# Optimization experiments

Hardware: AMD Instinct MI355X
Metric: run time of the kernel (lower is better)

## Reference

```python
import jax, jax.numpy as jnp
import numpy as np

NU, NM, E, H = 200000, 40000, 2000000, 64


def setup_inputs() -> dict:
    key = jax.random.key(0)
    ks = jax.random.split(key, 16)
    inp = {}
    inp["x_user"] = jnp.arange(NU, dtype=jnp.int32)
    inp["x_movie"] = jnp.arange(NM, dtype=jnp.int32)
    # user->movie ratings and the reverse edge type (same edges, flipped)
    src_u = jax.random.randint(ks[0], (E,), 0, NU, dtype=jnp.int32)
    dst_m = jax.random.randint(ks[1], (E,), 0, NM, dtype=jnp.int32)
    inp["edge_src_um"], inp["edge_dst_um"] = src_u, dst_m
    inp["edge_src_mu"], inp["edge_dst_mu"] = dst_m, src_u
    inp["user_table"] = jax.random.normal(ks[2], (NU, H), dtype=jnp.float32)
    inp["movie_table"] = jax.random.normal(ks[3], (NM, H), dtype=jnp.float32)
    s = 1.0 / np.sqrt(H)
    wnames = ["Wl1_um", "Wr1_um", "Wl1_mu", "Wr1_mu", "Wl2_um", "Wr2_um", "Wl2_mu", "Wr2_mu"]
    for i, n in enumerate(wnames):
        inp[n] = jax.random.uniform(ks[4 + i], (H, H), minval=-s, maxval=s, dtype=jnp.float32)
    for i, n in enumerate(["b1_um", "b1_mu", "b2_um", "b2_mu"]):
        inp[n] = jax.random.uniform(ks[12 + i], (H,), minval=-s, maxval=s, dtype=jnp.float32)
    return inp


def sage_conv(x_src, x_dst, src, dst, Wl, Wr, b, n_dst):
    """PyG SAGEConv (bipartite, aggr='mean'): lin_l(mean_j x_j) + lin_r(x_i) + b."""
    msg = x_src[src]                                            # [E, H] gather
    agg = jax.ops.segment_sum(msg, dst, num_segments=n_dst)     # [n_dst, H]
    cnt = jax.ops.segment_sum(jnp.ones((src.shape[0], 1), x_src.dtype), dst,
                              num_segments=n_dst)
    agg = agg / jnp.maximum(cnt, 1.0)                           # mean, 0 for isolated nodes
    return agg @ Wl + x_dst @ Wr + b


def reference(x_user, x_movie, edge_src_um, edge_dst_um, edge_src_mu, edge_dst_mu,
              user_table, movie_table,
              Wl1_um, Wr1_um, Wl1_mu, Wr1_mu, Wl2_um, Wr2_um, Wl2_mu, Wr2_mu,
              b1_um, b1_mu, b2_um, b2_mu):
    u0 = user_table[x_user]    # [NU, H]
    m0 = movie_table[x_movie]  # [NM, H]
    # layer 1 (per edge type; each node type has one incoming edge type, aggr='sum' trivial)
    m1 = jax.nn.relu(sage_conv(u0, m0, edge_src_um, edge_dst_um, Wl1_um, Wr1_um, b1_um, NM))
    u1 = jax.nn.relu(sage_conv(m0, u0, edge_src_mu, edge_dst_mu, Wl1_mu, Wr1_mu, b1_mu, NU))
    # layer 2
    m2 = sage_conv(u1, m1, edge_src_um, edge_dst_um, Wl2_um, Wr2_um, b2_um, NM)
    u2 = sage_conv(m1, u1, edge_src_mu, edge_dst_mu, Wl2_mu, Wr2_mu, b2_mu, NU)
    return (u2, m2)
```

## Files before the change

### kernel.cpp

```cpp
#include <hip/hip_runtime.h>

#define HDIM 64
#define CAP_M 96
#define CAP_U 32
#define OVF_MAX 65536

typedef __attribute__((ext_vector_type(8))) short bf16x8;
typedef __attribute__((ext_vector_type(4))) float f32x4;

__device__ __forceinline__ float bf2f(unsigned short u) {
  unsigned int x = ((unsigned int)u) << 16;
  return __uint_as_float(x);
}
__device__ __forceinline__ unsigned short f2bf(float f) {
  unsigned int x = __float_as_uint(f);
  unsigned int r = (x + 0x7FFFu + ((x >> 16) & 1u)) >> 16;
  return (unsigned short)r;
}

__global__ __launch_bounds__(256) void k_init(int* __restrict__ meta, int nmeta,
                                              const float* __restrict__ ut,
                                              unsigned short* __restrict__ ub, int n8u,
                                              const float* __restrict__ mt,
                                              unsigned short* __restrict__ mb, int n8m) {
  int bid = blockIdx.x;
  if (bid < 512) {
    int i = bid * 256 + threadIdx.x;
    for (int j = i; j < nmeta; j += 512 * 256) meta[j] = 0;
  } else if (bid < 512 + 2048) {
    int i = (bid - 512) * 256 + threadIdx.x;
    for (int j = i; j < n8u; j += 2048 * 256) {
      const float4* p = (const float4*)(ut + (size_t)j * 8);
      float4 a = p[0], b = p[1];
      uint4 o;
      o.x = (unsigned int)f2bf(a.x) | ((unsigned int)f2bf(a.y) << 16);
      o.y = (unsigned int)f2bf(a.z) | ((unsigned int)f2bf(a.w) << 16);
      o.z = (unsigned int)f2bf(b.x) | ((unsigned int)f2bf(b.y) << 16);
      o.w = (unsigned int)f2bf(b.z) | ((unsigned int)f2bf(b.w) << 16);
      *(uint4*)(ub + (size_t)j * 8) = o;
    }
  } else {
    int i = (bid - 512 - 2048) * 256 + threadIdx.x;
    for (int j = i; j < n8m; j += 512 * 256) {
      const float4* p = (const float4*)(mt + (size_t)j * 8);
      float4 a = p[0], b = p[1];
      uint4 o;
      o.x = (unsigned int)f2bf(a.x) | ((unsigned int)f2bf(a.y) << 16);
      o.y = (unsigned int)f2bf(a.z) | ((unsigned int)f2bf(a.w) << 16);
      o.z = (unsigned int)f2bf(b.x) | ((unsigned int)f2bf(b.y) << 16);
      o.w = (unsigned int)f2bf(b.z) | ((unsigned int)f2bf(b.w) << 16);
      *(uint4*)(mb + (size_t)j * 8) = o;
    }
  }
}

__global__ __launch_bounds__(256) void k_fillb2_x(const int* __restrict__ srcU,
                                                  const int* __restrict__ dstM,
                                                  int* __restrict__ curM,
                                                  int* __restrict__ bktM,
                                                  int* __restrict__ ovfM_cnt,
                                                  int* __restrict__ ovfM,
                                                  int* __restrict__ curU,
                                                  unsigned short* __restrict__ bktU,
                                                  int* __restrict__ ovfU_cnt,
                                                  int* __restrict__ ovfU,
                                                  int E, int NM_, int NU_) {
  int xg = blockIdx.x & 7;
  int mlo = (int)(((long long)NM_ * xg) >> 3);
  int mhi = (xg == 7) ? NM_ : (int)(((long long)NM_ * (xg + 1)) >> 3);
  int ulo = (int)(((long long)NU_ * xg) >> 3);
  int uhi = (xg == 7) ? NU_ : (int)(((long long)NU_ * (xg + 1)) >> 3);
  int li = (blockIdx.x >> 3) * blockDim.x + threadIdx.x;
  int stride = (gridDim.x >> 3) * blockDim.x;
  int E4 = E >> 2;
  const int4* s4 = (const int4*)srcU;
  const int4* d4 = (const int4*)dstM;
  for (int e = li; e < E4; e += stride) {
    int4 d = d4[e];
    int4 s = s4[e];
#pragma unroll
    for (int k = 0; k < 4; ++k) {
      int dd = (k == 0) ? d.x : (k == 1) ? d.y : (k == 2) ? d.z : d.w;
      int ss = (k == 0) ? s.x : (k == 1) ? s.y : (k == 2) ? s.z : s.w;
      if (dd >= mlo && dd < mhi) {
        int p = atomicAdd(&curM[dd], 1);
        if (p < CAP_M) bktM[(size_t)dd * CAP_M + p] = ss;
        else { int q = atomicAdd(ovfM_cnt, 1); if (q < OVF_MAX) { ovfM[2 * q] = dd; ovfM[2 * q + 1] = ss; } }
      }
      if (ss >= ulo && ss < uhi) {
        int p = atomicAdd(&curU[ss], 1);
        if (p < CAP_U) bktU[(size_t)ss * CAP_U + p] = (unsigned short)dd;
        else { int q = atomicAdd(ovfU_cnt, 1); if (q < OVF_MAX) { ovfU[2 * q] = ss; ovfU[2 * q + 1] = dd; } }
      }
    }
  }
  for (int e = E4 * 4 + li; e < E; e += stride) {
    int dd = dstM[e];
    int ss = srcU[e];
    if (dd >= mlo && dd < mhi) {
      int p = atomicAdd(&curM[dd], 1);
      if (p < CAP_M) bktM[(size_t)dd * CAP_M + p] = ss;
      else { int q = atomicAdd(ovfM_cnt, 1); if (q < OVF_MAX) { ovfM[2 * q] = dd; ovfM[2 * q + 1] = ss; } }
    }
    if (ss >= ulo && ss < uhi) {
      int p = atomicAdd(&curU[ss], 1);
      if (p < CAP_U) bktU[(size_t)ss * CAP_U + p] = (unsigned short)dd;
      else { int q = atomicAdd(ovfU_cnt, 1); if (q < OVF_MAX) { ovfU[2 * q] = ss; ovfU[2 * q + 1] = dd; } }
    }
  }
}

__device__ __forceinline__ void acc8(float4& a, float4& b, uint4 w) {
  a.x += __uint_as_float(w.x << 16);
  a.y += __uint_as_float(w.x & 0xFFFF0000u);
  a.z += __uint_as_float(w.y << 16);
  a.w += __uint_as_float(w.y & 0xFFFF0000u);
  b.x += __uint_as_float(w.z << 16);
  b.y += __uint_as_float(w.z & 0xFFFF0000u);
  b.z += __uint_as_float(w.w << 16);
  b.w += __uint_as_float(w.w & 0xFFFF0000u);
}

template <typename IT>
__global__ __launch_bounds__(256) void k_agg8(const unsigned short* __restrict__ xb,
                                              const int* __restrict__ cur,
                                              const IT* __restrict__ bkt,
                                              int cap,
                                              float* __restrict__ agg,
                                              int n_dst) {
  int t = threadIdx.x;
  int q = t & 7;
  int gg = (blockIdx.x * 256 + t) >> 3;
  int stride = (gridDim.x * 256) >> 3;

  for (int node = gg; node < n_dst; node += stride) {
    int deg = cur[node];
    int nb = deg < cap ? deg : cap;
    const IT* lst = bkt + (size_t)node * cap;
    float4 a = make_float4(0.f, 0.f, 0.f, 0.f);
    float4 b = a;
    int e = 0;
    for (; e + 4 <= nb; e += 4) {
      int i0, i1, i2, i3;
      if (sizeof(IT) == 2) {
        ushort4 ia = *(const ushort4*)&lst[e];
        i0 = ia.x; i1 = ia.y; i2 = ia.z; i3 = ia.w;
      } else {
        int4 ia = *(const int4*)&lst[e];
        i0 = ia.x; i1 = ia.y; i2 = ia.z; i3 = ia.w;
      }
      uint4 w0 = *(const uint4*)&xb[(size_t)i0 * HDIM + 8 * q];
      uint4 w1 = *(const uint4*)&xb[(size_t)i1 * HDIM + 8 * q];
      uint4 w2 = *(const uint4*)&xb[(size_t)i2 * HDIM + 8 * q];
      uint4 w3 = *(const uint4*)&xb[(size_t)i3 * HDIM + 8 * q];
      acc8(a, b, w0);
      acc8(a, b, w1);
      acc8(a, b, w2);
      acc8(a, b, w3);
    }
    for (; e < nb; ++e) {
      uint4 w0 = *(const uint4*)&xb[(size_t)lst[e] * HDIM + 8 * q];
      acc8(a, b, w0);
    }
    float inv = deg > 0 ? 1.f / (float)deg : 0.f;
    a.x *= inv; a.y *= inv; a.z *= inv; a.w *= inv;
    b.x *= inv; b.y *= inv; b.z *= inv; b.w *= inv;
    *(float4*)&agg[(size_t)node * HDIM + 8 * q] = a;
    *(float4*)&agg[(size_t)node * HDIM + 8 * q + 4] = b;
  }
}

__device__ __forceinline__ void fix_body(const int* __restrict__ cnt_p,
                                         const int* __restrict__ ovf,
                                         const unsigned short* __restrict__ xb,
                                         const int* __restrict__ cur,
                                         float* __restrict__ agg,
                                         int bid, int nblk) {
  int n = *cnt_p;
  if (n > OVF_MAX) n = OVF_MAX;
  int tid = bid * 256 + threadIdx.x;
  int q = tid & 15;
  int p = tid >> 4;
  int stride = (nblk * 256) >> 4;
  for (; p < n; p += stride) {
    int d = ovf[2 * p];
    int s = ovf[2 * p + 1];
    float inv = 1.f / (float)cur[d];
    ushort4 v = *(const ushort4*)&xb[(size_t)s * HDIM + 4 * q];
    atomicAdd(&agg[(size_t)d * HDIM + 4 * q + 0], bf2f(v.x) * inv);
    atomicAdd(&agg[(size_t)d * HDIM + 4 * q + 1], bf2f(v.y) * inv);
    atomicAdd(&agg[(size_t)d * HDIM + 4 * q + 2], bf2f(v.z) * inv);
    atomicAdd(&agg[(size_t)d * HDIM + 4 * q + 3], bf2f(v.w) * inv);
  }
}

__global__ __launch_bounds__(256) void k_fix2(const int* __restrict__ cntM,
                                              const int* __restrict__ ovfM,
                                              const unsigned short* __restrict__ xbM,
                                              const int* __restrict__ curM,
                                              float* __restrict__ aggM,
                                              const int* __restrict__ cntU,
                                              const int* __restrict__ ovfU,
                                              const unsigned short* __restrict__ xbU,
                                              const int* __restrict__ curU,
                                              float* __restrict__ aggU) {
  if (blockIdx.x < 16) fix_body(cntM, ovfM, xbM, curM, aggM, blockIdx.x, 16);
  else                 fix_body(cntU, ovfU, xbU, curU, aggU, blockIdx.x - 16, 16);
}

template <int OUTBF>
__global__ __launch_bounds__(256) void k_xmfma(const float* A,
                                               const unsigned short* X,
                                               const float* __restrict__ Wl,
                                               const float* __restrict__ Wr,
                                               const float* __restrict__ bias,
                                               void* outv,
                                               int n_dst, int do_relu) {
  __shared__ unsigned short sWt[64][136];
  __shared__ float sOut[4][16][68];

  int t = threadIdx.x;
  for (int id = t; id < 64 * 128; id += 256) {
    int col = id & 63;
    int k = id >> 6;
    float wv = (k < 64) ? Wl[k * 64 + col] : Wr[(k - 64) * 64 + col];
    sWt[col][k] = f2bf(wv);
  }
  __syncthreads();

  int w = t >> 6;
  int l = t & 63;
  int lm = l & 15;
  int lg = l >> 4;
  int wid = blockIdx.x * 4 + w;
  int nw = gridDim.x * 4;
  int ntiles = (n_dst + 15) >> 4;

  for (int tile = wid; tile < ntiles; tile += nw) {
    int nbase = tile << 4;
    int row = nbase + lm;
    int rowc = row < n_dst ? row : (n_dst - 1);

    bf16x8 afr[4];
    const float* ar = A + (size_t)rowc * HDIM;
#pragma unroll
    for (int s = 0; s < 2; ++s) {
      float4 f0 = *(const float4*)(ar + 32 * s + 8 * lg);
      float4 f1 = *(const float4*)(ar + 32 * s + 8 * lg + 4);
      bf16x8 v;
      v[0] = (short)f2bf(f0.x); v[1] = (short)f2bf(f0.y);
      v[2] = (short)f2bf(f0.z); v[3] = (short)f2bf(f0.w);
      v[4] = (short)f2bf(f1.x); v[5] = (short)f2bf(f1.y);
      v[6] = (short)f2bf(f1.z); v[7] = (short)f2bf(f1.w);
      afr[s] = v;
    }
    const unsigned short* xr = X + (size_t)rowc * HDIM;
#pragma unroll
    for (int s = 0; s < 2; ++s) {
      afr[2 + s] = *(const bf16x8*)(xr + 32 * s + 8 * lg);
    }

    f32x4 zz = {0.f, 0.f, 0.f, 0.f};
    f32x4 acc[4];
#pragma unroll
    for (int n = 0; n < 4; ++n) acc[n] = zz;
#pragma unroll
    for (int s = 0; s < 4; ++s) {
#pragma unroll
      for (int n = 0; n < 4; ++n) {
        bf16x8 bfr = *(const bf16x8*)(&sWt[16 * n + lm][32 * s + 8 * lg]);
        acc[n] = __builtin_amdgcn_mfma_f32_16x16x32_bf16(afr[s], bfr, acc[n], 0, 0, 0);
      }
    }

#pragma unroll
    for (int n = 0; n < 4; ++n) {
      float bj = bias[16 * n + lm];
#pragma unroll
      for (int r = 0; r < 4; ++r) {
        float v = acc[n][r] + bj;
        if (do_relu) v = fmaxf(v, 0.f);
        sOut[w][lg * 4 + r][16 * n + lm] = v;
      }
    }

    int node = nbase + (l >> 2);
    if (node < n_dst) {
      int c0 = (l & 3) * 16;
      float4 o0 = *(const float4*)&sOut[w][l >> 2][c0];
      float4 o1 = *(const float4*)&sOut[w][l >> 2][c0 + 4];
      float4 o2 = *(const float4*)&sOut[w][l >> 2][c0 + 8];
      float4 o3 = *(const float4*)&sOut[w][l >> 2][c0 + 12];
      if (OUTBF) {
        unsigned short* ob = (unsigned short*)outv;
        uint4 p0, p1;
        p0.x = (unsigned int)f2bf(o0.x) | ((unsigned int)f2bf(o0.y) << 16);
        p0.y = (unsigned int)f2bf(o0.z) | ((unsigned int)f2bf(o0.w) << 16);
        p0.z = (unsigned int)f2bf(o1.x) | ((unsigned int)f2bf(o1.y) << 16);
        p0.w = (unsigned int)f2bf(o1.z) | ((unsigned int)f2bf(o1.w) << 16);
        p1.x = (unsigned int)f2bf(o2.x) | ((unsigned int)f2bf(o2.y) << 16);
        p1.y = (unsigned int)f2bf(o2.z) | ((unsigned int)f2bf(o2.w) << 16);
        p1.z = (unsigned int)f2bf(o3.x) | ((unsigned int)f2bf(o3.y) << 16);
        p1.w = (unsigned int)f2bf(o3.z) | ((unsigned int)f2bf(o3.w) << 16);
        *(uint4*)&ob[(size_t)node * HDIM + c0] = p0;
        *(uint4*)&ob[(size_t)node * HDIM + c0 + 8] = p1;
      } else {
        float* of = (float*)outv;
        *(float4*)&of[(size_t)node * HDIM + c0] = o0;
        *(float4*)&of[(size_t)node * HDIM + c0 + 4] = o1;
        *(float4*)&of[(size_t)node * HDIM + c0 + 8] = o2;
        *(float4*)&of[(size_t)node * HDIM + c0 + 12] = o3;
      }
    }
  }
}


static inline int imin(int a, int b) { return a < b ? a : b; }

extern "C" void kernel_launch(void* const* d_in, const int* in_sizes, int n_in,
                              void* d_out, int out_size, void* d_ws, size_t ws_size,
                              hipStream_t stream) {
  const int NU = in_sizes[0];
  const int NM = in_sizes[1];
  const int E  = in_sizes[2];

  const int* src_um = (const int*)d_in[2];
  const int* dst_um = (const int*)d_in[3];
  const float* user_table  = (const float*)d_in[6];
  const float* movie_table = (const float*)d_in[7];
  const float* Wl1_um = (const float*)d_in[8];
  const float* Wr1_um = (const float*)d_in[9];
  const float* Wl1_mu = (const float*)d_in[10];
  const float* Wr1_mu = (const float*)d_in[11];
  const float* Wl2_um = (const float*)d_in[12];
  const float* Wr2_um = (const float*)d_in[13];
  const float* Wl2_mu = (const float*)d_in[14];
  const float* Wr2_mu = (const float*)d_in[15];
  const float* b1_um = (const float*)d_in[16];
  const float* b1_mu = (const float*)d_in[17];
  const float* b2_um = (const float*)d_in[18];
  const float* b2_mu = (const float*)d_in[19];

  float* out_u2 = (float*)d_out;
  float* out_m2 = (float*)d_out + (size_t)NU * HDIM;
  float* aggu = out_u2;
  float* aggm = out_m2;

  char* ws = (char*)d_ws;
  size_t off = 0;
  auto carve = [&](size_t bytes) -> char* {
    char* p = ws + off;
    off = (off + bytes + 255) & ~(size_t)255;
    return p;
  };
  int* meta = (int*)carve((size_t)(NM + NU + 2) * 4);
  int* curm = meta;
  int* curu = meta + NM;
  int* ovfm_cnt = meta + NM + NU;
  int* ovfu_cnt = meta + NM + NU + 1;
  int nmeta = NM + NU + 2;
  int* ovfm = (int*)carve((size_t)OVF_MAX * 2 * 4);
  int* ovfu = (int*)carve((size_t)OVF_MAX * 2 * 4);
  int* bktm = (int*)carve((size_t)NM * CAP_M * 4);
  unsigned short* bktu = (unsigned short*)carve((size_t)NU * CAP_U * 2);
  unsigned short* mb = (unsigned short*)carve((size_t)NM * HDIM * 2);
  unsigned short* ub = (unsigned short*)carve((size_t)NU * HDIM * 2);
  (void)ws_size;

  const int TB = 256;

  int n8u = NU * HDIM / 8, n8m = NM * HDIM / 8;
  k_init<<<3072, TB, 0, stream>>>(meta, nmeta, user_table, ub, n8u,
                                  movie_table, mb, n8m);

  k_fillb2_x<<<2048, TB, 0, stream>>>(src_um, dst_um,
                                      curm, bktm, ovfm_cnt, ovfm,
                                      curu, bktu, ovfu_cnt, ovfu,
                                      E, NM, NU);

  int gAm = imin((NM + 31) / 32, 8192);
  int gAu = imin((NU + 31) / 32, 8192);
  int gXm = (NM + 63) / 64;
  int gXu = (NU + 63) / 64;

  k_agg8<int><<<gAm, TB, 0, stream>>>(ub, curm, bktm, CAP_M, aggm, NM);
  k_agg8<unsigned short><<<gAu, TB, 0, stream>>>(mb, curu, bktu, CAP_U, aggu, NU);
  k_fix2<<<32, TB, 0, stream>>>(ovfm_cnt, ovfm, ub, curm, aggm,
                                ovfu_cnt, ovfu, mb, curu, aggu);
  k_xmfma<1><<<gXm, TB, 0, stream>>>(aggm, mb, Wl1_um, Wr1_um, b1_um,
                                     mb, NM, 1);
  k_xmfma<1><<<gXu, TB, 0, stream>>>(aggu, ub, Wl1_mu, Wr1_mu, b1_mu,
                                     ub, NU, 1);

  k_agg8<int><<<gAm, TB, 0, stream>>>(ub, curm, bktm, CAP_M, aggm, NM);
  k_agg8<unsigned short><<<gAu, TB, 0, stream>>>(mb, curu, bktu, CAP_U, aggu, NU);
  k_fix2<<<32, TB, 0, stream>>>(ovfm_cnt, ovfm, ub, curm, aggm,
                                ovfu_cnt, ovfu, mb, curu, aggu);
  k_xmfma<0><<<gXm, TB, 0, stream>>>(aggm, mb, Wl2_um, Wr2_um, b2_um,
                                     out_m2, NM, 0);
  k_xmfma<0><<<gXu, TB, 0, stream>>>(aggu, ub, Wl2_mu, Wr2_mu, b2_mu,
                                     out_u2, NU, 0);
}
```

Measured before the change: 420.2 us.

## Fuse neighbor aggregation with MFMA linear layers and recompute overflow nodes separately

Each SAGEConv becomes a single kernel. The kernel gathers bf16 neighbor rows per 16-row tile, forms the mean in registers, converts it to bf16 MFMA fragments and applies Wl/Wr plus bias directly. This removes the fp32 aggregate buffer round trip and the separate aggregate and GEMM launches. Nodes whose degree overflows the bucket capacity are now skipped in the fused kernel and fully recomputed by a new redo kernel, instead of being patched with atomics. Layer-1 outputs go to separate bf16 buffers, with a fallback path through scratch plus a final copy kernel when workspace is short. The cost is a per-node linear scan over the overflow list and less parallelism per node during the gather.

```diff
diff --git a/kernel.cpp b/kernel.cpp
--- a/kernel.cpp
+++ b/kernel.cpp
@@ -110,35 +110,57 @@
   }
 }
 
-__device__ __forceinline__ void acc8(float4& a, float4& b, uint4 w) {
-  a.x += __uint_as_float(w.x << 16);
-  a.y += __uint_as_float(w.x & 0xFFFF0000u);
-  a.z += __uint_as_float(w.y << 16);
-  a.w += __uint_as_float(w.y & 0xFFFF0000u);
-  b.x += __uint_as_float(w.z << 16);
-  b.y += __uint_as_float(w.z & 0xFFFF0000u);
-  b.z += __uint_as_float(w.w << 16);
-  b.w += __uint_as_float(w.w & 0xFFFF0000u);
-}
-
-template <typename IT>
-__global__ __launch_bounds__(256) void k_agg8(const unsigned short* __restrict__ xb,
-                                              const int* __restrict__ cur,
-                                              const IT* __restrict__ bkt,
-                                              int cap,
-                                              float* __restrict__ agg,
-                                              int n_dst) {
+template <typename IT, int OUTBF>
+__global__ __launch_bounds__(512) void k_sagex(const unsigned short* __restrict__ xg,
+                                               const int* __restrict__ cur,
+                                               const IT* __restrict__ bkt, int cap,
+                                               const int* __restrict__ ovf_cnt,
+                                               const int* __restrict__ ovf,
+                                               const unsigned short* __restrict__ X,
+                                               const float* __restrict__ Wl,
+                                               const float* __restrict__ Wr,
+                                               const float* __restrict__ bias,
+                                               void* outv, int n_dst, int do_relu) {
+  __shared__ unsigned short sWt[64][136];
+  __shared__ float sOut[8][16][68];
+
   int t = threadIdx.x;
-  int q = t & 7;
-  int gg = (blockIdx.x * 256 + t) >> 3;
-  int stride = (gridDim.x * 256) >> 3;
-
-  for (int node = gg; node < n_dst; node += stride) {
-    int deg = cur[node];
+  for (int id = t; id < 64 * 128; id += 512) {
+    int col = id & 63;
+    int k = id >> 6;
+    float wv = (k < 64) ? Wl[k * 64 + col] : Wr[(k - 64) * 64 + col];
+    sWt[col][k] = f2bf(wv);
+  }
+  __syncthreads();
+
+  int w = t >> 6;
+  int l = t & 63;
+  int lm = l & 15;
+  int lg = l >> 4;
+  int wid = blockIdx.x * 8 + w;
+  int nw = gridDim.x * 8;
+  int ntiles = (n_dst + 15) >> 4;
+  int novf = *ovf_cnt;
+  if (novf > OVF_MAX) novf = OVF_MAX;
+
+  for (int tile = wid; tile < ntiles; tile += nw) {
+    int nbase = tile << 4;
+    int row = nbase + lm;
+    int rowc = row < n_dst ? row : (n_dst - 1);
+    int deg = cur[rowc];
     int nb = deg < cap ? deg : cap;
-    const IT* lst = bkt + (size_t)node * cap;
-    float4 a = make_float4(0.f, 0.f, 0.f, 0.f);
-    float4 b = a;
+    const IT* lst = bkt + (size_t)rowc * cap;
+
+    float aA0=0,aA1=0,aA2=0,aA3=0,aA4=0,aA5=0,aA6=0,aA7=0;
+    float aB0=0,aB1=0,aB2=0,aB3=0,aB4=0,aB5=0,aB6=0,aB7=0;
+#define ADD8A(wv) { aA0+=__uint_as_float((wv).x<<16); aA1+=__uint_as_float((wv).x&0xFFFF0000u); \
+                    aA2+=__uint_as_float((wv).y<<16); aA3+=__uint_as_float((wv).y&0xFFFF0000u); \
+                    aA4+=__uint_as_float((wv).z<<16); aA5+=__uint_as_float((wv).z&0xFFFF0000u); \
+                    aA6+=__uint_as_float((wv).w<<16); aA7+=__uint_as_float((wv).w&0xFFFF0000u); }
+#define ADD8B(wv) { aB0+=__uint_as_float((wv).x<<16); aB1+=__uint_as_float((wv).x&0xFFFF0000u); \
+                    aB2+=__uint_as_float((wv).y<<16); aB3+=__uint_as_float((wv).y&0xFFFF0000u); \
+                    aB4+=__uint_as_float((wv).z<<16); aB5+=__uint_as_float((wv).z&0xFFFF0000u); \
+                    aB6+=__uint_as_float((wv).w<<16); aB7+=__uint_as_float((wv).w&0xFFFF0000u); }
     int e = 0;
     for (; e + 4 <= nb; e += 4) {
       int i0, i1, i2, i3;
@@ -149,116 +171,38 @@
         int4 ia = *(const int4*)&lst[e];
         i0 = ia.x; i1 = ia.y; i2 = ia.z; i3 = ia.w;
       }
-      uint4 w0 = *(const uint4*)&xb[(size_t)i0 * HDIM + 8 * q];
-      uint4 w1 = *(const uint4*)&xb[(size_t)i1 * HDIM + 8 * q];
-      uint4 w2 = *(const uint4*)&xb[(size_t)i2 * HDIM + 8 * q];
-      uint4 w3 = *(const uint4*)&xb[(size_t)i3 * HDIM + 8 * q];
-      acc8(a, b, w0);
-      acc8(a, b, w1);
-      acc8(a, b, w2);
-      acc8(a, b, w3);
+      uint4 p0 = *(const uint4*)&xg[(size_t)i0 * HDIM + 8 * lg];
+      uint4 q0 = *(const uint4*)&xg[(size_t)i0 * HDIM + 32 + 8 * lg];
+      uint4 p1 = *(const uint4*)&xg[(size_t)i1 * HDIM + 8 * lg];
+      uint4 q1 = *(const uint4*)&xg[(size_t)i1 * HDIM + 32 + 8 * lg];
+      uint4 p2 = *(const uint4*)&xg[(size_t)i2 * HDIM + 8 * lg];
+      uint4 q2 = *(const uint4*)&xg[(size_t)i2 * HDIM + 32 + 8 * lg];
+      uint4 p3 = *(const uint4*)&xg[(size_t)i3 * HDIM + 8 * lg];
+      uint4 q3 = *(const uint4*)&xg[(size_t)i3 * HDIM + 32 + 8 * lg];
+      ADD8A(p0); ADD8B(q0); ADD8A(p1); ADD8B(q1);
+      ADD8A(p2); ADD8B(q2); ADD8A(p3); ADD8B(q3);
     }
     for (; e < nb; ++e) {
-      uint4 w0 = *(const uint4*)&xb[(size_t)lst[e] * HDIM + 8 * q];
-      acc8(a, b, w0);
-    }
+      int i0 = (int)lst[e];
+      uint4 p0 = *(const uint4*)&xg[(size_t)i0 * HDIM + 8 * lg];
+      uint4 q0 = *(const uint4*)&xg[(size_t)i0 * HDIM + 32 + 8 * lg];
+      ADD8A(p0); ADD8B(q0);
+    }
+#undef ADD8A
+#undef ADD8B
+
     float inv = deg > 0 ? 1.f / (float)deg : 0.f;
-    a.x *= inv; a.y *= inv; a.z *= inv; a.w *= inv;
-    b.x *= inv; b.y *= inv; b.z *= inv; b.w *= inv;
-    *(float4*)&agg[(size_t)node * HDIM + 8 * q] = a;
-    *(float4*)&agg[(size_t)node * HDIM + 8 * q + 4] = b;
-  }
-}
-
-__device__ __forceinline__ void fix_body(const int* __restrict__ cnt_p,
-                                         const int* __restrict__ ovf,
-                                         const unsigned short* __restrict__ xb,
-                                         const int* __restrict__ cur,
-                                         float* __restrict__ agg,
-                                         int bid, int nblk) {
-  int n = *cnt_p;
-  if (n > OVF_MAX) n = OVF_MAX;
-  int tid = bid * 256 + threadIdx.x;
-  int q = tid & 15;
-  int p = tid >> 4;
-  int stride = (nblk * 256) >> 4;
-  for (; p < n; p += stride) {
-    int d = ovf[2 * p];
-    int s = ovf[2 * p + 1];
-    float inv = 1.f / (float)cur[d];
-    ushort4 v = *(const ushort4*)&xb[(size_t)s * HDIM + 4 * q];
-    atomicAdd(&agg[(size_t)d * HDIM + 4 * q + 0], bf2f(v.x) * inv);
-    atomicAdd(&agg[(size_t)d * HDIM + 4 * q + 1], bf2f(v.y) * inv);
-    atomicAdd(&agg[(size_t)d * HDIM + 4 * q + 2], bf2f(v.z) * inv);
-    atomicAdd(&agg[(size_t)d * HDIM + 4 * q + 3], bf2f(v.w) * inv);
-  }
-}
-
-__global__ __launch_bounds__(256) void k_fix2(const int* __restrict__ cntM,
-                                              const int* __restrict__ ovfM,
-                                              const unsigned short* __restrict__ xbM,
-                                              const int* __restrict__ curM,
-                                              float* __restrict__ aggM,
-                                              const int* __restrict__ cntU,
-                                              const int* __restrict__ ovfU,
-                                              const unsigned short* __restrict__ xbU,
-                                              const int* __restrict__ curU,
-                                              float* __restrict__ aggU) {
-  if (blockIdx.x < 16) fix_body(cntM, ovfM, xbM, curM, aggM, blockIdx.x, 16);
-  else                 fix_body(cntU, ovfU, xbU, curU, aggU, blockIdx.x - 16, 16);
-}
-
-template <int OUTBF>
-__global__ __launch_bounds__(256) void k_xmfma(const float* A,
-                                               const unsigned short* X,
-                                               const float* __restrict__ Wl,
-                                               const float* __restrict__ Wr,
-                                               const float* __restrict__ bias,
-                                               void* outv,
-                                               int n_dst, int do_relu) {
-  __shared__ unsigned short sWt[64][136];
-  __shared__ float sOut[4][16][68];
-
-  int t = threadIdx.x;
-  for (int id = t; id < 64 * 128; id += 256) {
-    int col = id & 63;
-    int k = id >> 6;
-    float wv = (k < 64) ? Wl[k * 64 + col] : Wr[(k - 64) * 64 + col];
-    sWt[col][k] = f2bf(wv);
-  }
-  __syncthreads();
-
-  int w = t >> 6;
-  int l = t & 63;
-  int lm = l & 15;
-  int lg = l >> 4;
-  int wid = blockIdx.x * 4 + w;
-  int nw = gridDim.x * 4;
-  int ntiles = (n_dst + 15) >> 4;
-
-  for (int tile = wid; tile < ntiles; tile += nw) {
-    int nbase = tile << 4;
-    int row = nbase + lm;
-    int rowc = row < n_dst ? row : (n_dst - 1);
-
-    bf16x8 afr[4];
-    const float* ar = A + (size_t)rowc * HDIM;
-#pragma unroll
-    for (int s = 0; s < 2; ++s) {
-      float4 f0 = *(const float4*)(ar + 32 * s + 8 * lg);
-      float4 f1 = *(const float4*)(ar + 32 * s + 8 * lg + 4);
-      bf16x8 v;
-      v[0] = (short)f2bf(f0.x); v[1] = (short)f2bf(f0.y);
-      v[2] = (short)f2bf(f0.z); v[3] = (short)f2bf(f0.w);
-      v[4] = (short)f2bf(f1.x); v[5] = (short)f2bf(f1.y);
-      v[6] = (short)f2bf(f1.z); v[7] = (short)f2bf(f1.w);
-      afr[s] = v;
-    }
-    const unsigned short* xr = X + (size_t)rowc * HDIM;
-#pragma unroll
-    for (int s = 0; s < 2; ++s) {
-      afr[2 + s] = *(const bf16x8*)(xr + 32 * s + 8 * lg);
-    }
+    bf16x8 afr0, afr1;
+    afr0[0] = (short)f2bf(aA0 * inv); afr0[1] = (short)f2bf(aA1 * inv);
+    afr0[2] = (short)f2bf(aA2 * inv); afr0[3] = (short)f2bf(aA3 * inv);
+    afr0[4] = (short)f2bf(aA4 * inv); afr0[5] = (short)f2bf(aA5 * inv);
+    afr0[6] = (short)f2bf(aA6 * inv); afr0[7] = (short)f2bf(aA7 * inv);
+    afr1[0] = (short)f2bf(aB0 * inv); afr1[1] = (short)f2bf(aB1 * inv);
+    afr1[2] = (short)f2bf(aB2 * inv); afr1[3] = (short)f2bf(aB3 * inv);
+    afr1[4] = (short)f2bf(aB4 * inv); afr1[5] = (short)f2bf(aB5 * inv);
+    afr1[6] = (short)f2bf(aB6 * inv); afr1[7] = (short)f2bf(aB7 * inv);
+    bf16x8 afr2 = *(const bf16x8*)&X[(size_t)rowc * HDIM + 8 * lg];
+    bf16x8 afr3 = *(const bf16x8*)&X[(size_t)rowc * HDIM + 32 + 8 * lg];
 
     f32x4 zz = {0.f, 0.f, 0.f, 0.f};
     f32x4 acc[4];
@@ -266,10 +210,11 @@
     for (int n = 0; n < 4; ++n) acc[n] = zz;
 #pragma unroll
     for (int s = 0; s < 4; ++s) {
+      bf16x8 af = (s == 0) ? afr0 : (s == 1) ? afr1 : (s == 2) ? afr2 : afr3;
 #pragma unroll
       for (int n = 0; n < 4; ++n) {
         bf16x8 bfr = *(const bf16x8*)(&sWt[16 * n + lm][32 * s + 8 * lg]);
-        acc[n] = __builtin_amdgcn_mfma_f32_16x16x32_bf16(afr[s], bfr, acc[n], 0, 0, 0);
+        acc[n] = __builtin_amdgcn_mfma_f32_16x16x32_bf16(af, bfr, acc[n], 0, 0, 0);
       }
     }
 
@@ -285,7 +230,12 @@
     }
 
     int node = nbase + (l >> 2);
-    if (node < n_dst) {
+    bool skip = false;
+    if (novf > 0) {
+      for (int j2 = 0; j2 < novf; ++j2)
+        if (ovf[2 * j2] == node) { skip = true; break; }
+    }
+    if (node < n_dst && !skip) {
       int c0 = (l & 3) * 16;
       float4 o0 = *(const float4*)&sOut[w][l >> 2][c0];
       float4 o1 = *(const float4*)&sOut[w][l >> 2][c0 + 4];
@@ -315,6 +265,85 @@
   }
 }
 
+__device__ __forceinline__ void redo_side(const int* cnt_p, const int* ovf,
+                                          const unsigned short* g, const int* cur,
+                                          const void* bkt, int cap, int is16,
+                                          const unsigned short* X,
+                                          const float* Wl, const float* Wr,
+                                          const float* bb, void* out, int obf,
+                                          int relu, int bq, float* in) {
+  int n = *cnt_p;
+  if (n > OVF_MAX) n = OVF_MAX;
+  if (n == 0) return;
+  int t = threadIdx.x;
+  for (int q = bq; q < n; q += 32) {
+    int d = ovf[2 * q];
+    if (t < 64) {
+      float s = 0.f;
+      int deg = cur[d];
+      int nb = deg < cap ? deg : cap;
+      for (int j = 0; j < nb; ++j) {
+        int idx = is16 ? (int)((const unsigned short*)bkt)[(size_t)d * cap + j]
+                       : ((const int*)bkt)[(size_t)d * cap + j];
+        s += bf2f(g[(size_t)idx * HDIM + t]);
+      }
+      for (int j = 0; j < n; ++j)
+        if (ovf[2 * j] == d) s += bf2f(g[(size_t)ovf[2 * j + 1] * HDIM + t]);
+      in[t] = s / (float)deg;
+      in[64 + t] = bf2f(X[(size_t)d * HDIM + t]);
+    }
+    __syncthreads();
+    if (t < 64) {
+      float o = bb[t];
+      for (int k = 0; k < 64; ++k) o += in[k] * Wl[k * 64 + t];
+      for (int k = 0; k < 64; ++k) o += in[64 + k] * Wr[k * 64 + t];
+      if (relu) o = fmaxf(o, 0.f);
+      if (obf) ((unsigned short*)out)[(size_t)d * HDIM + t] = f2bf(o);
+      else ((float*)out)[(size_t)d * HDIM + t] = o;
+    }
+    __syncthreads();
+  }
+}
+
+__global__ __launch_bounds__(128) void k_redo(
+    const int* cM, const int* oM, const unsigned short* gM, const int* curM,
+    const void* bM, int capM, const unsigned short* XM,
+    const float* WlM, const float* WrM, const float* bbM, void* outM, int obfM, int reluM,
+    const int* cU, const int* oU, const unsigned short* gU, const int* curU,
+    const void* bU, int capU, const unsigned short* XU,
+    const float* WlU, const float* WrU, const float* bbU, void* outU, int obfU, int reluU) {
+  __shared__ float in[128];
+  int b = blockIdx.x;
+  if (b < 32)
+    redo_side(cM, oM, gM, curM, bM, capM, 0, XM, WlM, WrM, bbM, outM, obfM, reluM, b, in);
+  else
+    redo_side(cU, oU, gU, curU, bU, capU, 1, XU, WlU, WrU, bbU, outU, obfU, reluU, b - 32, in);
+}
+
+__global__ __launch_bounds__(256) void k_final(const unsigned short* __restrict__ ubuf,
+                                               const float* __restrict__ mscr,
+                                               float* __restrict__ dout,
+                                               int NUn, int NMn) {
+  int i = blockIdx.x * 256 + threadIdx.x;
+  int stride = gridDim.x * 256;
+  int nu8 = NUn * HDIM / 8;
+  for (int j = i; j < nu8; j += stride) {
+    uint4 v = *(const uint4*)&ubuf[(size_t)j * 8];
+    float4 f0, f1;
+    f0.x = __uint_as_float(v.x << 16); f0.y = __uint_as_float(v.x & 0xFFFF0000u);
+    f0.z = __uint_as_float(v.y << 16); f0.w = __uint_as_float(v.y & 0xFFFF0000u);
+    f1.x = __uint_as_float(v.z << 16); f1.y = __uint_as_float(v.z & 0xFFFF0000u);
+    f1.z = __uint_as_float(v.w << 16); f1.w = __uint_as_float(v.w & 0xFFFF0000u);
+    *(float4*)&dout[(size_t)j * 8] = f0;
+    *(float4*)&dout[(size_t)j * 8 + 4] = f1;
+  }
+  float* m2 = dout + (size_t)NUn * HDIM;
+  int nm4 = NMn * HDIM / 4;
+  for (int j = i; j < nm4; j += stride) {
+    *(float4*)&m2[(size_t)j * 4] = *(const float4*)&mscr[(size_t)j * 4];
+  }
+}
+
 
 static inline int imin(int a, int b) { return a < b ? a : b; }
 
@@ -344,8 +373,6 @@
 
   float* out_u2 = (float*)d_out;
   float* out_m2 = (float*)d_out + (size_t)NU * HDIM;
-  float* aggu = out_u2;
-  float* aggm = out_m2;
 
   char* ws = (char*)d_ws;
   size_t off = 0;
@@ -366,39 +393,65 @@
   unsigned short* bktu = (unsigned short*)carve((size_t)NU * CAP_U * 2);
   unsigned short* mb = (unsigned short*)carve((size_t)NM * HDIM * 2);
   unsigned short* ub = (unsigned short*)carve((size_t)NU * HDIM * 2);
-  (void)ws_size;
+
+  size_t m1sz = (((size_t)NM * HDIM * 2) + 255) & ~(size_t)255;
+  size_t u1sz = (((size_t)NU * HDIM * 2) + 255) & ~(size_t)255;
+  bool pathA = (off + m1sz + u1sz) <= ws_size;
+
+  unsigned short *m1b, *u1b, *ubuf = 0;
+  float* mscr = 0;
+  if (pathA) {
+    m1b = (unsigned short*)carve((size_t)NM * HDIM * 2);
+    u1b = (unsigned short*)carve((size_t)NU * HDIM * 2);
+  } else {
+    u1b = (unsigned short*)d_out;
+    m1b = (unsigned short*)((char*)d_out + (size_t)NU * 256);
+    mscr = (float*)carve((size_t)NM * HDIM * 4);
+    ubuf = ub;
+  }
 
   const int TB = 256;
 
   int n8u = NU * HDIM / 8, n8m = NM * HDIM / 8;
   k_init<<<3072, TB, 0, stream>>>(meta, nmeta, user_table, ub, n8u,
                                   movie_table, mb, n8m);
-
   k_fillb2_x<<<2048, TB, 0, stream>>>(src_um, dst_um,
                                       curm, bktm, ovfm_cnt, ovfm,
                                       curu, bktu, ovfu_cnt, ovfu,
                                       E, NM, NU);
 
-  int gAm = imin((NM + 31) / 32, 8192);
-  int gAu = imin((NU + 31) / 32, 8192);
-  int gXm = (NM + 63) / 64;
-  int gXu = (NU + 63) / 64;
-
-  k_agg8<int><<<gAm, TB, 0, stream>>>(ub, curm, bktm, CAP_M, aggm, NM);
-  k_agg8<unsigned short><<<gAu, TB, 0, stream>>>(mb, curu, bktu, CAP_U, aggu, NU);
-  k_fix2<<<32, TB, 0, stream>>>(ovfm_cnt, ovfm, ub, curm, aggm,
-                                ovfu_cnt, ovfu, mb, curu, aggu);
-  k_xmfma<1><<<gXm, TB, 0, stream>>>(aggm, mb, Wl1_um, Wr1_um, b1_um,
-                                     mb, NM, 1);
-  k_xmfma<1><<<gXu, TB, 0, stream>>>(aggu, ub, Wl1_mu, Wr1_mu, b1_mu,
-                                     ub, NU, 1);
-
-  k_agg8<int><<<gAm, TB, 0, stream>>>(ub, curm, bktm, CAP_M, aggm, NM);
-  k_agg8<unsigned short><<<gAu, TB, 0, stream>>>(mb, curu, bktu, CAP_U, aggu, NU);
-  k_fix2<<<32, TB, 0, stream>>>(ovfm_cnt, ovfm, ub, curm, aggm,
-                                ovfu_cnt, ovfu, mb, curu, aggu);
-  k_xmfma<0><<<gXm, TB, 0, stream>>>(aggm, mb, Wl2_um, Wr2_um, b2_um,
-                                     out_m2, NM, 0);
-  k_xmfma<0><<<gXu, TB, 0, stream>>>(aggu, ub, Wl2_mu, Wr2_mu, b2_mu,
-                                     out_u2, NU, 0);
-}
+  int gM = (NM + 127) / 128;
+  int gU = (NU + 127) / 128;
+
+  k_sagex<int, 1><<<gM, 512, 0, stream>>>(ub, curm, bktm, CAP_M, ovfm_cnt, ovfm,
+                                          mb, Wl1_um, Wr1_um, b1_um, m1b, NM, 1);
+  k_sagex<unsigned short, 1><<<gU, 512, 0, stream>>>(mb, curu, bktu, CAP_U, ovfu_cnt, ovfu,
+                                                     ub, Wl1_mu, Wr1_mu, b1_mu, u1b, NU, 1);
+  k_redo<<<64, 128, 0, stream>>>(ovfm_cnt, ovfm, ub, curm, bktm, CAP_M, mb,
+                                 Wl1_um, Wr1_um, b1_um, m1b, 1, 1,
+                                 ovfu_cnt, ovfu, mb, curu, bktu, CAP_U, ub,
+                                 Wl1_mu, Wr1_mu, b1_mu, u1b, 1, 1);
+
+  void* m2dst = pathA ? (void*)out_m2 : (void*)mscr;
+  void* u2dst = pathA ? (void*)out_u2 : (void*)ubuf;
+  k_redo<<<64, 128, 0, stream>>>(ovfm_cnt, ovfm, u1b, curm, bktm, CAP_M, m1b,
+                                 Wl2_um, Wr2_um, b2_um, m2dst, 0, 0,
+                                 ovfu_cnt, ovfu, m1b, curu, bktu, CAP_U, u1b,
+                                 Wl2_mu, Wr2_mu, b2_mu, u2dst, pathA ? 0 : 1, 0);
+  if (pathA) {
+    k_sagex<unsigned short, 0><<<gU, 512, 0, stream>>>(m1b, curu, bktu, CAP_U, ovfu_cnt, ovfu,
+                                                       u1b, Wl2_mu, Wr2_mu, b2_mu,
+                                                       out_u2, NU, 0);
+    k_sagex<int, 0><<<gM, 512, 0, stream>>>(u1b, curm, bktm, CAP_M, ovfm_cnt, ovfm,
+                                            m1b, Wl2_um, Wr2_um, b2_um,
+                                            out_m2, NM, 0);
+  } else {
+    k_sagex<unsigned short, 1><<<gU, 512, 0, stream>>>(m1b, curu, bktu, CAP_U, ovfu_cnt, ovfu,
+                                                       u1b, Wl2_mu, Wr2_mu, b2_mu,
+                                                       ubuf, NU, 0);
+    k_sagex<int, 0><<<gM, 512, 0, stream>>>(u1b, curm, bktm, CAP_M, ovfm_cnt, ovfm,
+                                            m1b, Wl2_um, Wr2_um, b2_um,
+                                            mscr, NM, 0);
+    k_final<<<2048, TB, 0, stream>>>(ubuf, mscr, (float*)d_out, NU, NM);
+  }
+}
```

After: 477.1 us. 13.6% more time.

## Replace global-atomic bucket fill with two-pass radix binning and LDS-local fills

Applied to the files above, without the earlier changes.

Replaces the single bucket-fill kernel, which did global atomics on per-node counters, with a pipeline per edge direction: a block histogram over 512 coarse bins, a prefix scan, a scatter of (key,value) pairs into binned order, and a per-bin fill that uses LDS counters and writes node buckets locally. The aim is to replace scattered global atomics with LDS atomics and give the bucket writes better locality. In exchange it adds about a dozen extra launches and an extra write and read of the binned 16 MB pair array, which is staged in the output buffer. k_fillbin's LDS counter array holds 400 entries, which is enough for 40000/512 and 200000/512 nodes per bin.

```diff
diff --git a/kernel.cpp b/kernel.cpp
--- a/kernel.cpp
+++ b/kernel.cpp
@@ -4,6 +4,7 @@
 #define CAP_M 96
 #define CAP_U 32
 #define OVF_MAX 65536
+#define NBIN 512
 
 typedef __attribute__((ext_vector_type(8))) short bf16x8;
 typedef __attribute__((ext_vector_type(4))) float f32x4;
@@ -54,60 +55,163 @@
   }
 }
 
-__global__ __launch_bounds__(256) void k_fillb2_x(const int* __restrict__ srcU,
-                                                  const int* __restrict__ dstM,
-                                                  int* __restrict__ curM,
-                                                  int* __restrict__ bktM,
-                                                  int* __restrict__ ovfM_cnt,
-                                                  int* __restrict__ ovfM,
-                                                  int* __restrict__ curU,
-                                                  unsigned short* __restrict__ bktU,
-                                                  int* __restrict__ ovfU_cnt,
-                                                  int* __restrict__ ovfU,
-                                                  int E, int NM_, int NU_) {
-  int xg = blockIdx.x & 7;
-  int mlo = (int)(((long long)NM_ * xg) >> 3);
-  int mhi = (xg == 7) ? NM_ : (int)(((long long)NM_ * (xg + 1)) >> 3);
-  int ulo = (int)(((long long)NU_ * xg) >> 3);
-  int uhi = (xg == 7) ? NU_ : (int)(((long long)NU_ * (xg + 1)) >> 3);
-  int li = (blockIdx.x >> 3) * blockDim.x + threadIdx.x;
-  int stride = (gridDim.x >> 3) * blockDim.x;
-  int E4 = E >> 2;
-  const int4* s4 = (const int4*)srcU;
-  const int4* d4 = (const int4*)dstM;
-  for (int e = li; e < E4; e += stride) {
-    int4 d = d4[e];
-    int4 s = s4[e];
-#pragma unroll
-    for (int k = 0; k < 4; ++k) {
-      int dd = (k == 0) ? d.x : (k == 1) ? d.y : (k == 2) ? d.z : d.w;
-      int ss = (k == 0) ? s.x : (k == 1) ? s.y : (k == 2) ? s.z : s.w;
-      if (dd >= mlo && dd < mhi) {
-        int p = atomicAdd(&curM[dd], 1);
-        if (p < CAP_M) bktM[(size_t)dd * CAP_M + p] = ss;
-        else { int q = atomicAdd(ovfM_cnt, 1); if (q < OVF_MAX) { ovfM[2 * q] = dd; ovfM[2 * q + 1] = ss; } }
+__global__ __launch_bounds__(256) void k_hist(const int* __restrict__ keys, int E, int Nd,
+                                              int* __restrict__ gh) {
+  __shared__ int h[NBIN];
+  int t = threadIdx.x;
+  h[t] = 0; h[t + 256] = 0;
+  __syncthreads();
+  int e4 = (E + 3) >> 2;
+  int c4 = (e4 + NBIN - 1) >> 9;
+  int clen = c4 << 2;
+  int s = blockIdx.x * clen;
+  int epos = s + clen; if (epos > E) epos = E;
+  for (int i = s + 4 * t; i < epos; i += 1024) {
+    int n = epos - i; if (n > 4) n = 4;
+    if (n == 4) {
+      int4 k4 = *(const int4*)&keys[i];
+      atomicAdd(&h[(int)((long long)k4.x * NBIN / Nd)], 1);
+      atomicAdd(&h[(int)((long long)k4.y * NBIN / Nd)], 1);
+      atomicAdd(&h[(int)((long long)k4.z * NBIN / Nd)], 1);
+      atomicAdd(&h[(int)((long long)k4.w * NBIN / Nd)], 1);
+    } else {
+      for (int j = 0; j < n; ++j)
+        atomicAdd(&h[(int)((long long)keys[i + j] * NBIN / Nd)], 1);
+    }
+  }
+  __syncthreads();
+  gh[(size_t)t * NBIN + blockIdx.x] = h[t];
+  gh[(size_t)(t + 256) * NBIN + blockIdx.x] = h[t + 256];
+}
+
+__global__ void k_block_sum(const int* __restrict__ in, int* __restrict__ part, int n) {
+  __shared__ int s[256];
+  int b = blockIdx.x, t = threadIdx.x;
+  int base = b * 1024;
+  int v = 0;
+  for (int i = t; i < 1024; i += 256) {
+    int idx = base + i;
+    if (idx < n) v += in[idx];
+  }
+  s[t] = v;
+  __syncthreads();
+  for (int o = 128; o > 0; o >>= 1) {
+    if (t < o) s[t] += s[t + o];
+    __syncthreads();
+  }
+  if (t == 0) part[b] = s[0];
+}
+
+__global__ void k_scan_part(int* __restrict__ part, int nb) {
+  __shared__ int s[256];
+  int t = threadIdx.x;
+  int v = (t < nb) ? part[t] : 0;
+  s[t] = v;
+  __syncthreads();
+  for (int o = 1; o < 256; o <<= 1) {
+    int u = (t >= o) ? s[t - o] : 0;
+    __syncthreads();
+    s[t] += u;
+    __syncthreads();
+  }
+  if (t < nb) part[t] = s[t] - v;
+}
+
+__global__ void k_scan_final(const int* __restrict__ in, const int* __restrict__ part,
+                             int* __restrict__ out, int n) {
+  __shared__ int s[256];
+  int b = blockIdx.x, t = threadIdx.x;
+  int base = b * 1024 + t * 4;
+  int a[4];
+#pragma unroll
+  for (int i = 0; i < 4; i++) a[i] = (base + i < n) ? in[base + i] : 0;
+  int tsum = a[0] + a[1] + a[2] + a[3];
+  s[t] = tsum;
+  __syncthreads();
+  for (int o = 1; o < 256; o <<= 1) {
+    int u = (t >= o) ? s[t - o] : 0;
+    __syncthreads();
+    s[t] += u;
+    __syncthreads();
+  }
+  int excl = s[t] - tsum + part[b];
+#pragma unroll
+  for (int i = 0; i < 4; i++) {
+    if (base + i < n) out[base + i] = excl;
+    excl += a[i];
+  }
+}
+
+__global__ __launch_bounds__(256) void k_scatter(const int* __restrict__ keys,
+                                                 const int* __restrict__ vals,
+                                                 int E, int Nd,
+                                                 const int* __restrict__ offs,
+                                                 int2* __restrict__ binned) {
+  __shared__ int lcur[NBIN];
+  int t = threadIdx.x;
+  lcur[t] = offs[(size_t)t * NBIN + blockIdx.x];
+  lcur[t + 256] = offs[(size_t)(t + 256) * NBIN + blockIdx.x];
+  __syncthreads();
+  int e4 = (E + 3) >> 2;
+  int c4 = (e4 + NBIN - 1) >> 9;
+  int clen = c4 << 2;
+  int s = blockIdx.x * clen;
+  int epos = s + clen; if (epos > E) epos = E;
+  for (int i = s + 4 * t; i < epos; i += 1024) {
+    int n = epos - i; if (n > 4) n = 4;
+    if (n == 4) {
+      int4 k4 = *(const int4*)&keys[i];
+      int4 v4 = *(const int4*)&vals[i];
+      int b0 = (int)((long long)k4.x * NBIN / Nd);
+      int b1 = (int)((long long)k4.y * NBIN / Nd);
+      int b2 = (int)((long long)k4.z * NBIN / Nd);
+      int b3 = (int)((long long)k4.w * NBIN / Nd);
+      int p0 = atomicAdd(&lcur[b0], 1);
+      int p1 = atomicAdd(&lcur[b1], 1);
+      int p2 = atomicAdd(&lcur[b2], 1);
+      int p3 = atomicAdd(&lcur[b3], 1);
+      binned[p0] = make_int2(k4.x, v4.x);
+      binned[p1] = make_int2(k4.y, v4.y);
+      binned[p2] = make_int2(k4.z, v4.z);
+      binned[p3] = make_int2(k4.w, v4.w);
+    } else {
+      for (int j = 0; j < n; ++j) {
+        int k = keys[i + j], v = vals[i + j];
+        int bb = (int)((long long)k * NBIN / Nd);
+        int p = atomicAdd(&lcur[bb], 1);
+        binned[p] = make_int2(k, v);
       }
-      if (ss >= ulo && ss < uhi) {
-        int p = atomicAdd(&curU[ss], 1);
-        if (p < CAP_U) bktU[(size_t)ss * CAP_U + p] = (unsigned short)dd;
-        else { int q = atomicAdd(ovfU_cnt, 1); if (q < OVF_MAX) { ovfU[2 * q] = ss; ovfU[2 * q + 1] = dd; } }
-      }
-    }
-  }
-  for (int e = E4 * 4 + li; e < E; e += stride) {
-    int dd = dstM[e];
-    int ss = srcU[e];
-    if (dd >= mlo && dd < mhi) {
-      int p = atomicAdd(&curM[dd], 1);
-      if (p < CAP_M) bktM[(size_t)dd * CAP_M + p] = ss;
-      else { int q = atomicAdd(ovfM_cnt, 1); if (q < OVF_MAX) { ovfM[2 * q] = dd; ovfM[2 * q + 1] = ss; } }
-    }
-    if (ss >= ulo && ss < uhi) {
-      int p = atomicAdd(&curU[ss], 1);
-      if (p < CAP_U) bktU[(size_t)ss * CAP_U + p] = (unsigned short)dd;
-      else { int q = atomicAdd(ovfU_cnt, 1); if (q < OVF_MAX) { ovfU[2 * q] = ss; ovfU[2 * q + 1] = dd; } }
-    }
-  }
+    }
+  }
+}
+
+template <typename IT>
+__global__ __launch_bounds__(256) void k_fillbin(const int2* __restrict__ binned,
+                                                 const int* __restrict__ offs,
+                                                 int E, int Nd, int cap,
+                                                 IT* __restrict__ bkt,
+                                                 int* __restrict__ cur,
+                                                 int* __restrict__ ovf_cnt,
+                                                 int* __restrict__ ovf) {
+  __shared__ int lcur[400];
+  int b = blockIdx.x;
+  int t = threadIdx.x;
+  int lo = (int)(((long long)b * Nd + NBIN - 1) >> 9);
+  int hi = (int)(((long long)(b + 1) * Nd + NBIN - 1) >> 9);
+  int width = hi - lo;
+  for (int i = t; i < width; i += 256) lcur[i] = 0;
+  __syncthreads();
+  int start = offs[b << 9];
+  int end = (b == NBIN - 1) ? E : offs[(b + 1) << 9];
+  for (int i = start + t; i < end; i += 256) {
+    int2 p = binned[i];
+    int li = p.x - lo;
+    int pos = atomicAdd(&lcur[li], 1);
+    if (pos < cap) bkt[(size_t)p.x * cap + pos] = (IT)p.y;
+    else { int q = atomicAdd(ovf_cnt, 1); if (q < OVF_MAX) { ovf[2 * q] = p.x; ovf[2 * q + 1] = p.y; } }
+  }
+  __syncthreads();
+  for (int i = t; i < width; i += 256) cur[lo + i] = lcur[i];
 }
 
 __device__ __forceinline__ void acc8(float4& a, float4& b, uint4 w) {
@@ -346,6 +450,7 @@
   float* out_m2 = (float*)d_out + (size_t)NU * HDIM;
   float* aggu = out_u2;
   float* aggm = out_m2;
+  int2* binned = (int2*)d_out;
 
   char* ws = (char*)d_ws;
   size_t off = 0;
@@ -366,18 +471,34 @@
   unsigned short* bktu = (unsigned short*)carve((size_t)NU * CAP_U * 2);
   unsigned short* mb = (unsigned short*)carve((size_t)NM * HDIM * 2);
   unsigned short* ub = (unsigned short*)carve((size_t)NU * HDIM * 2);
+  int* gh  = (int*)carve((size_t)NBIN * NBIN * 4);
+  int* ghs = (int*)carve((size_t)NBIN * NBIN * 4);
+  int* part = (int*)carve(256 * 4);
   (void)ws_size;
 
   const int TB = 256;
+  int nscan = NBIN * NBIN;
+  int nbscan = (nscan + 1023) / 1024;
 
   int n8u = NU * HDIM / 8, n8m = NM * HDIM / 8;
   k_init<<<3072, TB, 0, stream>>>(meta, nmeta, user_table, ub, n8u,
                                   movie_table, mb, n8m);
 
-  k_fillb2_x<<<2048, TB, 0, stream>>>(src_um, dst_um,
-                                      curm, bktm, ovfm_cnt, ovfm,
-                                      curu, bktu, ovfu_cnt, ovfu,
-                                      E, NM, NU);
+  k_hist<<<NBIN, TB, 0, stream>>>(dst_um, E, NM, gh);
+  k_block_sum<<<nbscan, TB, 0, stream>>>(gh, part, nscan);
+  k_scan_part<<<1, TB, 0, stream>>>(part, nbscan);
+  k_scan_final<<<nbscan, TB, 0, stream>>>(gh, part, ghs, nscan);
+  k_scatter<<<NBIN, TB, 0, stream>>>(dst_um, src_um, E, NM, ghs, binned);
+  k_fillbin<int><<<NBIN, TB, 0, stream>>>(binned, ghs, E, NM, CAP_M,
+                                          bktm, curm, ovfm_cnt, ovfm);
+
+  k_hist<<<NBIN, TB, 0, stream>>>(src_um, E, NU, gh);
+  k_block_sum<<<nbscan, TB, 0, stream>>>(gh, part, nscan);
+  k_scan_part<<<1, TB, 0, stream>>>(part, nbscan);
+  k_scan_final<<<nbscan, TB, 0, stream>>>(gh, part, ghs, nscan);
+  k_scatter<<<NBIN, TB, 0, stream>>>(src_um, dst_um, E, NU, ghs, binned);
+  k_fillbin<unsigned short><<<NBIN, TB, 0, stream>>>(binned, ghs, E, NU, CAP_U,
+                                                     bktu, curu, ovfu_cnt, ovfu);
 
   int gAm = imin((NM + 31) / 32, 8192);
   int gAu = imin((NU + 31) / 32, 8192);
```

Result: faster. 349.4 us (-16.8%).
